# Optimization experiments

Hardware: AMD Instinct MI355X
Metric: run time of the kernel (lower is better)

The kernel has to match this reference:

```python
import jax, jax.numpy as jnp
import numpy as np

B, N = 8, 2000                  # images, proposals per image
NUM_CLASSES = 91                # incl. background (class 0)
IMG_H, IMG_W = 800, 1333
SCORE_THRESH = 0.05
NMS_THRESH = 0.5
DETS_PER_IMG = 100
PRE_NMS_TOPK = 2048             # fixed-size cap on NMS candidates (jit-static)
MIN_SIZE = 0.01
WX, WY, WW, WH = 10.0, 10.0, 5.0, 5.0   # BoxCoder weights
BBOX_XFORM_CLIP = float(np.log(1000.0 / 16.0))


def setup_inputs() -> dict:
    key = jax.random.key(0)
    k1, k2, k3, k4 = jax.random.split(key, 4)
    # valid proposal boxes (x1,y1,x2,y2) inside the image
    ctr = jax.random.uniform(k1, (B, N, 2)) * jnp.array([IMG_W, IMG_H], jnp.float32)
    wh = jax.random.uniform(k2, (B, N, 2), minval=8.0, maxval=256.0)
    proposals = jnp.concatenate([ctr - 0.5 * wh, ctr + 0.5 * wh], axis=-1)
    class_logits = jax.random.normal(k3, (B * N, NUM_CLASSES)) * 2.0
    box_regression = jax.random.normal(k4, (B * N, NUM_CLASSES * 4)) * 0.2
    return {"class_logits": class_logits, "box_regression": box_regression,
            "proposals": proposals}


def _decode(reg, boxes):
    # reg: [N, C, 4] deltas, boxes: [N, 4] proposals -> [N, C, 4] decoded
    w = boxes[:, 2] - boxes[:, 0]
    h = boxes[:, 3] - boxes[:, 1]
    cx = boxes[:, 0] + 0.5 * w
    cy = boxes[:, 1] + 0.5 * h
    dx = reg[..., 0] / WX
    dy = reg[..., 1] / WY
    dw = jnp.minimum(reg[..., 2] / WW, BBOX_XFORM_CLIP)
    dh = jnp.minimum(reg[..., 3] / WH, BBOX_XFORM_CLIP)
    pcx = dx * w[:, None] + cx[:, None]
    pcy = dy * h[:, None] + cy[:, None]
    pw = jnp.exp(dw) * w[:, None]
    ph = jnp.exp(dh) * h[:, None]
    return jnp.stack([pcx - 0.5 * pw, pcy - 0.5 * ph,
                      pcx + 0.5 * pw, pcy + 0.5 * ph], axis=-1)


def _box_iou(a, b):
    # a: [K,4], b: [K,4] -> [K,K]
    area_a = (a[:, 2] - a[:, 0]) * (a[:, 3] - a[:, 1])
    area_b = (b[:, 2] - b[:, 0]) * (b[:, 3] - b[:, 1])
    lt = jnp.maximum(a[:, None, :2], b[None, :, :2])
    rb = jnp.minimum(a[:, None, 2:], b[None, :, 2:])
    wh = jnp.clip(rb - lt, 0.0)
    inter = wh[..., 0] * wh[..., 1]
    return inter / (area_a[:, None] + area_b[None, :] - inter)


def _postprocess_image(boxes, scores):
    # boxes: [N, C, 4] decoded, scores: [N, C] softmax probs
    boxes = jnp.stack([jnp.clip(boxes[..., 0], 0.0, IMG_W),
                       jnp.clip(boxes[..., 1], 0.0, IMG_H),
                       jnp.clip(boxes[..., 2], 0.0, IMG_W),
                       jnp.clip(boxes[..., 3], 0.0, IMG_H)], axis=-1)
    # drop background class 0, flatten to per-(proposal,class) candidates
    boxes_fg = boxes[:, 1:, :].reshape(-1, 4)            # [N*(C-1), 4]
    scores_fg = scores[:, 1:].reshape(-1)
    labels_fg = jnp.broadcast_to(jnp.arange(1, NUM_CLASSES, dtype=jnp.int32),
                                 (N, NUM_CLASSES - 1)).reshape(-1)
    ws = boxes_fg[:, 2] - boxes_fg[:, 0]
    hs = boxes_fg[:, 3] - boxes_fg[:, 1]
    valid = (scores_fg > SCORE_THRESH) & (ws >= MIN_SIZE) & (hs >= MIN_SIZE)
    # fixed-size pre-NMS top-K (masked-out candidates sorted last)
    _, top_idx = jax.lax.top_k(jnp.where(valid, scores_fg, -1.0), PRE_NMS_TOPK)
    cand_boxes = boxes_fg[top_idx]
    cand_scores = scores_fg[top_idx]
    cand_labels = labels_fg[top_idx]
    cand_valid = valid[top_idx]
    # class-wise (batched) NMS via per-class coordinate offset
    offset = cand_labels.astype(cand_boxes.dtype) * (jnp.max(cand_boxes) + 1.0)
    iou = _box_iou(cand_boxes + offset[:, None], cand_boxes + offset[:, None])
    idx = jnp.arange(PRE_NMS_TOPK)

    def body(i, keep):  # greedy suppression in score order
        sup = (iou[i] > NMS_THRESH) & keep[i] & (idx > i)
        return keep & ~sup

    keep = jax.lax.fori_loop(0, PRE_NMS_TOPK, body, cand_valid)
    out_scores, out_idx = jax.lax.top_k(jnp.where(keep, cand_scores, -1.0),
                                        DETS_PER_IMG)
    return cand_boxes[out_idx], out_scores, cand_labels[out_idx]


def reference(class_logits, box_regression, proposals):
    logits = class_logits.reshape(B, N, NUM_CLASSES)
    reg = box_regression.reshape(B, N, NUM_CLASSES, 4)
    pred_boxes = jax.vmap(_decode)(reg, proposals)          # [B, N, C, 4]
    pred_scores = jax.nn.softmax(logits, axis=-1)           # [B, N, C]
    boxes, scores, labels = jax.vmap(_postprocess_image)(pred_boxes, pred_scores)
    return boxes, scores, labels
```

## Files before the change

kernel.cpp:

```cpp
#include <hip/hip_runtime.h>
#include <cstdint>
#include <cstddef>

#define NIMG   8
#define NPROP  2000
#define NCLS   91
#define NFG    90
#define NROW   (NIMG * NPROP)
#define TOPK   2048
#define DETS   100
#define CKCAP  32768
#define KREGS  12
#define CLSCAP 512

#define IMG_Wf 1333.0f
#define IMG_Hf 800.0f
#define SCORE_TH 0.05f
#define MINSZ    0.01f
#define NMS_TH   0.5f
#define CLIPV    4.135166556742356f
#define ORD_NEG1 0x407FFFFFu
#define PADKEY   (((ull)ORD_NEG1 << 32) | 0xFFFFFFFFull)

typedef unsigned long long ull;

static const size_t OFF_CNT    = 0;
static const size_t OFF_KBM    = 2048;
static const size_t OFF_VBM    = 4096;
static const size_t OFF_CK     = 262144;
static const size_t OFF_CBOX   = OFF_CK    + (size_t)NIMG*CKCAP*8;
static const size_t OFF_CSCOR  = OFF_CBOX  + (size_t)NIMG*TOPK*16;
static const size_t OFF_CLAB   = OFF_CSCOR + (size_t)NIMG*TOPK*4;
static const size_t OFF_CLSBOX = OFF_CLAB  + (size_t)NIMG*TOPK*4;
static const size_t OFF_CLSAR  = OFF_CLSBOX+ (size_t)NIMG*TOPK*16;
static const size_t OFF_CLSSX  = OFF_CLSAR + (size_t)NIMG*TOPK*4;
static const size_t OFF_CLSCNT = OFF_CLSSX + (size_t)NIMG*TOPK*4;
static const size_t OFF_CLSOFF = OFF_CLSCNT+ (size_t)NIMG*96*4;

__device__ __forceinline__ unsigned ford(float f) {
    unsigned u = __float_as_uint(f);
    return (u & 0x80000000u) ? ~u : (u | 0x80000000u);
}
__device__ __forceinline__ float fordinv(unsigned x) {
    return (x & 0x80000000u) ? __uint_as_float(x & 0x7FFFFFFFu)
                             : __uint_as_float(~x);
}

__device__ __forceinline__ float4 decode_clip(float4 p, float4 r) {
    float w  = __fsub_rn(p.z, p.x);
    float h  = __fsub_rn(p.w, p.y);
    float cx = __fadd_rn(p.x, __fmul_rn(0.5f, w));
    float cy = __fadd_rn(p.y, __fmul_rn(0.5f, h));
    float dx = __fdiv_rn(r.x, 10.0f);
    float dy = __fdiv_rn(r.y, 10.0f);
    float dw = fminf(__fdiv_rn(r.z, 5.0f), CLIPV);
    float dh = fminf(__fdiv_rn(r.w, 5.0f), CLIPV);
    float pcx = __fadd_rn(__fmul_rn(dx, w), cx);
    float pcy = __fadd_rn(__fmul_rn(dy, h), cy);
    float pw  = __fmul_rn(expf(dw), w);
    float ph  = __fmul_rn(expf(dh), h);
    float x1 = __fsub_rn(pcx, __fmul_rn(0.5f, pw));
    float y1 = __fsub_rn(pcy, __fmul_rn(0.5f, ph));
    float x2 = __fadd_rn(pcx, __fmul_rn(0.5f, pw));
    float y2 = __fadd_rn(pcy, __fmul_rn(0.5f, ph));
    float4 o;
    o.x = fminf(fmaxf(x1, 0.0f), IMG_Wf);
    o.y = fminf(fmaxf(y1, 0.0f), IMG_Hf);
    o.z = fminf(fmaxf(x2, 0.0f), IMG_Wf);
    o.w = fminf(fmaxf(y2, 0.0f), IMG_Hf);
    return o;
}

__device__ __forceinline__ void wl_phase(ull& a, ull& b, int l, int base,
                                         int k, int jmax) {
    bool desc = ((base & k) == 0);
    for (int j = jmax; j >= 2; j >>= 1) {
        int pl = l ^ (j >> 1);
        bool lower = ((base & j) == 0);
        ull pa = __shfl(a, pl), pb = __shfl(b, pl);
        bool km = (desc == lower);
        ull na = km ? (a > pa ? a : pa) : (a < pa ? a : pa);
        ull nb = km ? (b > pb ? b : pb) : (b < pb ? b : pb);
        a = na; b = nb;
    }
    ull mx = a > b ? a : b, mn = a > b ? b : a;
    a = desc ? mx : mn; b = desc ? mn : mx;
}

__global__ __launch_bounds__(1024) void kA(const float* __restrict__ logits,
                                           const float* __restrict__ reg,
                                           const float* __restrict__ props,
                                           ull* __restrict__ ck,
                                           int* __restrict__ cntv,
                                           ull* __restrict__ vbm2) {
    int warp = threadIdx.x >> 6;
    int lane = threadIdx.x & 63;
    int row  = blockIdx.x * 16 + warp;
    int b = row / NPROP;
    int n = row - b * NPROP;
    const float* lrow = logits + (size_t)row * NCLS;

    float xa = lrow[lane];
    float xb = (lane < 27) ? lrow[64 + lane] : -INFINITY;
    float mx = fmaxf(xa, xb);
    #pragma unroll
    for (int o = 32; o; o >>= 1) mx = fmaxf(mx, __shfl_xor(mx, o));
    float ea = expf(__fsub_rn(xa, mx));
    float eb = (lane < 27) ? expf(__fsub_rn(xb, mx)) : 0.0f;
    float s  = __fadd_rn(ea, eb);
    #pragma unroll
    for (int o = 32; o; o >>= 1) s = __fadd_rn(s, __shfl_xor(s, o));

    const float4 p = *reinterpret_cast<const float4*>(props + (size_t)row * 4);

    __shared__ int sCnt[32];
    __shared__ int sExc[32];
    __shared__ int sBase;

    ull rowmask[2];
    bool validA[2];
    ull keyA[2];
    #pragma unroll
    for (int it = 0; it < 2; ++it) {
        int c = (it == 0) ? (1 + lane) : (65 + lane);
        bool active = (it == 0) ? true : (lane < 26);
        bool valid = false;
        ull key = 0;
        if (active) {
            float lg = lrow[c];
            float score = __fdiv_rn(expf(__fsub_rn(lg, mx)), s);
            float4 r4 = *reinterpret_cast<const float4*>(
                reg + ((size_t)row * NCLS + c) * 4);
            float4 bx = decode_clip(p, r4);
            float bw = __fsub_rn(bx.z, bx.x);
            float bh = __fsub_rn(bx.w, bx.y);
            valid = (score > SCORE_TH) && (bw >= MINSZ) && (bh >= MINSZ);
            int offidx = n * NFG + (c - 1);
            key = ((ull)ford(score) << 32) |
                  (ull)(0xFFFFFFFFu - (unsigned)offidx);
        }
        ull bal = __ballot(valid);
        rowmask[it] = bal;
        validA[it] = valid;
        keyA[it] = key;
        if (lane == 0) sCnt[warp * 2 + it] = __popcll(bal);
    }
    __syncthreads();
    if (warp == 0) {
        int c = (lane < 32) ? sCnt[lane] : 0;
        int p2 = c;
        #pragma unroll
        for (int o = 1; o < 32; o <<= 1) {
            int v = __shfl_up(p2, o);
            if (lane >= o) p2 += v;
        }
        if (lane == 31) sBase = atomicAdd(&cntv[b * 64], p2);
        if (lane < 32) sExc[lane] = p2 - c;
    }
    __syncthreads();
    int base = sBase;
    #pragma unroll
    for (int it = 0; it < 2; ++it) {
        if (validA[it]) {
            int slot = base + sExc[warp * 2 + it] +
                       __popcll(rowmask[it] & ((1ull << lane) - 1ull));
            if (slot < CKCAP)
                ck[(size_t)b * CKCAP + slot] = keyA[it];
        }
    }
    if (lane == 0) {
        vbm2[(size_t)row * 2]     = rowmask[0];
        vbm2[(size_t)row * 2 + 1] = rowmask[1];
    }
}

__global__ __launch_bounds__(1024) void kB(const ull* __restrict__ ck,
                                           const int* __restrict__ cntv,
                                           const ull* __restrict__ vbm2,
                                           const float* __restrict__ reg,
                                           const float* __restrict__ props,
                                           float4* __restrict__ cbox,
                                           float* __restrict__ cscore,
                                           int* __restrict__ clabel,
                                           float4* __restrict__ clsbox,
                                           float* __restrict__ clsarea,
                                           int* __restrict__ clssidx,
                                           int* __restrict__ clscnt,
                                           int* __restrict__ clsoff) {
    int b = blockIdx.x;
    int tid = threadIdx.x;
    int lane = tid & 63, warp = tid >> 6;
    __shared__ ull sk[TOPK];
    __shared__ unsigned histw[16 * 256];
    __shared__ unsigned wtot4[4];
    __shared__ ull sP;
    __shared__ int sRem, sCnt;
    __shared__ float sMax[16];
    __shared__ float sM1;
    __shared__ int rex[NPROP];
    __shared__ int wsum[16];
    __shared__ ull clsbm[NFG * 32];
    __shared__ unsigned wpfx[NFG * 32];
    __shared__ int ccnt[96], coff[96];

    int cnt = cntv[b * 64];
    if (cnt > CKCAP) cnt = CKCAP;
    const ull* K = ck + (size_t)b * CKCAP;

    if (cnt >= TOPK) {
        ull kreg[KREGS];
        #pragma unroll
        for (int r = 0; r < KREGS; ++r) {
            int i = tid + (r << 10);
            kreg[r] = (i < cnt) ? K[i] : 0ull;
        }
        ull P = 0; int rem = TOPK;
        for (int pass = 7; pass >= 0; --pass) {
            int sh = pass * 8;
            *reinterpret_cast<uint4*>(&histw[tid * 4]) = make_uint4(0, 0, 0, 0);
            __syncthreads();
            ull pmask = (pass == 7) ? 0ull : (~0ull << (sh + 8));
            unsigned* hw = &histw[warp << 8];
            #pragma unroll
            for (int r = 0; r < KREGS; ++r) {
                int i = tid + (r << 10);
                if (i < cnt && (kreg[r] & pmask) == P)
                    atomicAdd(&hw[(unsigned)(kreg[r] >> sh) & 255u], 1u);
            }
            for (int i = (KREGS << 10) + tid; i < cnt; i += 1024) {
                ull k2 = K[i];
                if ((k2 & pmask) == P)
                    atomicAdd(&hw[(unsigned)(k2 >> sh) & 255u], 1u);
            }
            __syncthreads();
            unsigned x = 0, pfx = 0;
            if (tid < 256) {
                int d = 255 - tid;
                #pragma unroll
                for (int w = 0; w < 16; ++w) x += histw[(w << 8) + d];
                pfx = x;
                #pragma unroll
                for (int o = 1; o < 64; o <<= 1) {
                    unsigned v = __shfl_up(pfx, o);
                    if (lane >= o) pfx += v;
                }
                if (lane == 63) wtot4[tid >> 6] = pfx;
            }
            __syncthreads();
            if (tid < 256) {
                int d = 255 - tid;
                int ws = tid >> 6;
                unsigned add = 0;
                if (ws > 0) add += wtot4[0];
                if (ws > 1) add += wtot4[1];
                if (ws > 2) add += wtot4[2];
                unsigned pi   = pfx + add;
                unsigned excl = pi - x;
                if (x && excl < (unsigned)rem && pi >= (unsigned)rem) {
                    sP = P | ((ull)(unsigned)d << sh);
                    sRem = rem - (int)excl;
                }
            }
            __syncthreads();
            P = sP; rem = sRem;
        }
        if (tid == 0) sCnt = 0;
        __syncthreads();
        #pragma unroll
        for (int r = 0; r < KREGS; ++r) {
            int i = tid + (r << 10);
            bool sel = (i < cnt) && (kreg[r] >= P);
            ull bal = __ballot(sel);
            int cw = __popcll(bal);
            if (cw) {
                int ldr = __ffsll((long long)bal) - 1;
                int bw = 0;
                if (lane == ldr) bw = atomicAdd(&sCnt, cw);
                bw = __shfl(bw, ldr);
                if (sel) {
                    int pos = bw + __popcll(bal & ((1ull << lane) - 1ull));
                    if (pos < TOPK) sk[pos] = kreg[r];
                }
            }
        }
        for (int i = (KREGS << 10) + tid; i < cnt; i += 1024) {
            ull k2 = K[i];
            bool sel = (k2 >= P);
            ull bal = __ballot(sel);
            int cw = __popcll(bal);
            if (cw) {
                int ldr = __ffsll((long long)bal) - 1;
                int bw = 0;
                if (lane == ldr) bw = atomicAdd(&sCnt, cw);
                bw = __shfl(bw, ldr);
                if (sel) {
                    int pos = bw + __popcll(bal & ((1ull << lane) - 1ull));
                    if (pos < TOPK) sk[pos] = k2;
                }
            }
        }
        __syncthreads();
        int fc = sCnt;
        for (int i = fc + tid; i < TOPK; i += 1024) sk[i] = PADKEY;
    } else {
        for (int i = tid; i < cnt; i += 1024) sk[i] = K[i];
        int F = TOPK - cnt;
        const ull* V = vbm2 + (size_t)b * NPROP * 2;
        int r0 = 2 * tid, r1 = r0 + 1;
        int v0 = 0, v1 = 0;
        if (r0 < NPROP) v0 = NFG - __popcll(V[r0 * 2]) - __popcll(V[r0 * 2 + 1]);
        if (r1 < NPROP) v1 = NFG - __popcll(V[r1 * 2]) - __popcll(V[r1 * 2 + 1]);
        int s2 = v0 + v1;
        int pfx = s2;
        #pragma unroll
        for (int o = 1; o < 64; o <<= 1) {
            int t = __shfl_up(pfx, o);
            if (lane >= o) pfx += t;
        }
        if (lane == 63) wsum[warp] = pfx;
        __syncthreads();
        if (tid == 0) {
            int a = 0;
            for (int w = 0; w < 16; ++w) { int t = wsum[w]; wsum[w] = a; a += t; }
        }
        __syncthreads();
        int excl = pfx - s2 + wsum[warp];
        if (r0 < NPROP) rex[r0] = excl;
        if (r1 < NPROP) rex[r1] = excl + v0;
        __syncthreads();
        for (int r = tid; r < NPROP; r += 1024) {
            int e = rex[r];
            if (e < F) {
                ull m0 = V[r * 2], m1 = V[r * 2 + 1];
                int rank = e;
                ull inv = ~m0;
                while (inv && rank < F) {
                    int cb = __builtin_ctzll(inv); inv &= inv - 1;
                    unsigned idx = (unsigned)(r * NFG + cb);
                    sk[cnt + rank] = ((ull)ORD_NEG1 << 32) | (ull)(0xFFFFFFFFu - idx);
                    ++rank;
                }
                inv = (~m1) & ((1ull << 26) - 1ull);
                while (inv && rank < F) {
                    int cb = __builtin_ctzll(inv); inv &= inv - 1;
                    unsigned idx = (unsigned)(r * NFG + 64 + cb);
                    sk[cnt + rank] = ((ull)ORD_NEG1 << 32) | (ull)(0xFFFFFFFFu - idx);
                    ++rank;
                }
            }
        }
    }
    __syncthreads();

    {
        int ebase = warp * 128 + lane * 2;
        ulonglong2 v = *reinterpret_cast<ulonglong2*>(&sk[ebase]);
        ull a = v.x, bb = v.y;
        #pragma unroll
        for (int k = 2; k <= 128; k <<= 1)
            wl_phase(a, bb, lane, ebase, k, (k >> 1) < 64 ? (k >> 1) : 64);
        v.x = a; v.y = bb;
        *reinterpret_cast<ulonglong2*>(&sk[ebase]) = v;
        for (int k = 256; k <= TOPK; k <<= 1) {
            for (int j = k >> 1; j >= 128; j >>= 1) {
                __syncthreads();
                for (int i = tid; i < TOPK; i += 1024) {
                    int ij = i ^ j;
                    if (ij > i) {
                        ull x1 = sk[i], x2 = sk[ij];
                        bool descSeg = ((i & k) == 0);
                        if ((x1 < x2) == descSeg) { sk[i] = x2; sk[ij] = x1; }
                    }
                }
            }
            __syncthreads();
            v = *reinterpret_cast<ulonglong2*>(&sk[ebase]);
            a = v.x; bb = v.y;
            wl_phase(a, bb, lane, ebase, k, 64);
            v.x = a; v.y = bb;
            *reinterpret_cast<ulonglong2*>(&sk[ebase]) = v;
        }
    }
    __syncthreads();

    float lmax = 0.0f;
    float4 myb[2]; int myl[2]; float mys[2]; bool vkA[2];
    #pragma unroll
    for (int r = 0; r < 2; ++r) {
        int sidx = tid + r * 1024;
        ull k = sk[sidx];
        unsigned idx = 0xFFFFFFFFu - (unsigned)(k & 0xFFFFFFFFu);
        float score = fordinv((unsigned)(k >> 32));
        int n = (int)(idx / NFG), c = (int)(idx % NFG);
        int row = b * NPROP + n;
        float4 p  = *reinterpret_cast<const float4*>(props + (size_t)row * 4);
        float4 r4 = *reinterpret_cast<const float4*>(
            reg + ((size_t)row * NCLS + (c + 1)) * 4);
        float4 bx = decode_clip(p, r4);
        myb[r] = bx; myl[r] = c + 1; mys[r] = score;
        vkA[r] = (((unsigned)(k >> 32)) != ORD_NEG1);
        lmax = fmaxf(lmax, fmaxf(fmaxf(bx.x, bx.y), fmaxf(bx.z, bx.w)));
    }
    #pragma unroll
    for (int o = 32; o; o >>= 1) lmax = fmaxf(lmax, __shfl_xor(lmax, o));
    if ((tid & 63) == 0) sMax[tid >> 6] = lmax;
    __syncthreads();
    if (tid == 0) {
        float v = sMax[0];
        for (int i = 1; i < 16; ++i) v = fmaxf(v, sMax[i]);
        sM1 = __fadd_rn(v, 1.0f);
    }
    __syncthreads();
    float m1 = sM1;
    float4 obA[2]; float arA[2];
    #pragma unroll
    for (int r = 0; r < 2; ++r) {
        int sidx = tid + r * 1024;
        float off = __fmul_rn((float)myl[r], m1);
        float4 ob;
        ob.x = __fadd_rn(myb[r].x, off);
        ob.y = __fadd_rn(myb[r].y, off);
        ob.z = __fadd_rn(myb[r].z, off);
        ob.w = __fadd_rn(myb[r].w, off);
        float area = __fmul_rn(__fsub_rn(ob.z, ob.x), __fsub_rn(ob.w, ob.y));
        obA[r] = ob; arA[r] = area;
        int g = b * TOPK + sidx;
        cbox[g] = myb[r]; cscore[g] = mys[r]; clabel[g] = myl[r];
    }

    for (int i = tid; i < NFG * 32; i += 1024) clsbm[i] = 0ull;
    __syncthreads();
    #pragma unroll
    for (int r = 0; r < 2; ++r) {
        int sidx = tid + (r << 10);
        if (vkA[r])
            atomicOr(&clsbm[(myl[r] - 1) * 32 + (sidx >> 6)], 1ull << (sidx & 63));
    }
    __syncthreads();
    if (tid < NFG) {
        unsigned run = 0;
        for (int w = 0; w < 32; ++w) {
            wpfx[tid * 32 + w] = run;
            run += (unsigned)__popcll(clsbm[tid * 32 + w]);
        }
        ccnt[tid] = (int)run;
    }
    __syncthreads();
    if (tid == 0) {
        int a = 0;
        for (int c2 = 0; c2 < NFG; ++c2) { coff[c2] = a; a += ccnt[c2]; }
    }
    __syncthreads();
    #pragma unroll
    for (int r = 0; r < 2; ++r) {
        int sidx = tid + (r << 10);
        if (vkA[r]) {
            int cl = myl[r] - 1;
            int rank = (int)wpfx[cl * 32 + (sidx >> 6)] +
                       (int)__popcll(clsbm[cl * 32 + (sidx >> 6)] &
                                     ((1ull << (sidx & 63)) - 1ull));
            int slot = coff[cl] + rank;
            int g2 = b * TOPK + slot;
            clsbox[g2] = obA[r]; clsarea[g2] = arA[r]; clssidx[g2] = sidx;
        }
    }
    if (tid < NFG) {
        clscnt[b * 96 + tid] = ccnt[tid];
        clsoff[b * 96 + tid] = coff[tid];
    }
}

__global__ __launch_bounds__(64) void kN(const float4* __restrict__ clsbox,
                                         const float* __restrict__ clsarea,
                                         const int* __restrict__ clssidx,
                                         const int* __restrict__ clscnt,
                                         const int* __restrict__ clsoff,
                                         ull* __restrict__ keepbm) {
    int bc = blockIdx.x;
    int b = bc / NFG, c = bc - b * NFG;
    int n = clscnt[b * 96 + c];
    if (n <= 0) return;
    if (n > CLSCAP) n = CLSCAP;
    int lane = threadIdx.x;
    int W = (n + 63) >> 6;
    __shared__ float4 sbox[CLSCAP];
    __shared__ float  sar[CLSCAP];
    __shared__ int    ssx[CLSCAP];
    __shared__ ull    smask[CLSCAP * 8];
    int base = b * TOPK + clsoff[b * 96 + c];
    for (int t = lane; t < n; t += 64) {
        sbox[t] = clsbox[base + t];
        sar[t]  = clsarea[base + t];
        ssx[t]  = clssidx[base + t];
    }
    __syncthreads();
    for (int i = lane; i < n; i += 64) {
        float4 a = sbox[i]; float ai = sar[i];
        for (int w = 0; w < W; ++w) {
            ull word = 0;
            int jn = n - (w << 6); if (jn > 64) jn = 64;
            for (int s = 0; s < jn; ++s) {
                int j = (w << 6) + s;
                if (j > i) {
                    float4 cc = sbox[j];
                    float lt0 = fmaxf(a.x, cc.x), lt1 = fmaxf(a.y, cc.y);
                    float rb0 = fminf(a.z, cc.z), rb1 = fminf(a.w, cc.w);
                    float w0 = fmaxf(__fsub_rn(rb0, lt0), 0.0f);
                    float w1 = fmaxf(__fsub_rn(rb1, lt1), 0.0f);
                    float inter = __fmul_rn(w0, w1);
                    if (inter > 0.0f) {
                        float un = __fsub_rn(__fadd_rn(ai, sar[j]), inter);
                        if (__fdiv_rn(inter, un) > NMS_TH) word |= (1ull << s);
                    }
                }
            }
            smask[i * W + w] = word;
        }
    }
    __syncthreads();
    ull alive = 0;
    if (lane < W) {
        int rem = n - (lane << 6);
        alive = (rem >= 64) ? ~0ull : ((1ull << rem) - 1ull);
    }
    for (int i = 0; i < n; ++i) {
        ull aw = __shfl(alive, i >> 6);
        if ((aw >> (i & 63)) & 1ull) {
            if (lane < W) alive &= ~smask[i * W + lane];
        }
    }
    if (lane < W) {
        ull bits = alive;
        while (bits) {
            int s = __builtin_ctzll(bits); bits &= bits - 1;
            int sidx = ssx[(lane << 6) + s];
            atomicOr(&keepbm[b * 32 + (sidx >> 6)], 1ull << (sidx & 63));
        }
    }
}

__global__ __launch_bounds__(64) void kE(const ull* __restrict__ keepbm,
                                         const float4* __restrict__ cbox,
                                         const float* __restrict__ cscore,
                                         const int* __restrict__ clabel,
                                         float* __restrict__ out) {
    int b = blockIdx.x;
    int lane = threadIdx.x;
    __shared__ ull sKeep[32];
    if (lane < 32) sKeep[lane] = keepbm[b * 32 + lane];
    __syncthreads();

    unsigned m = (unsigned)(sKeep[lane >> 1] >> ((lane & 1) << 5));

    int cntk = __popc(m);
    int pre = cntk;
    #pragma unroll
    for (int o = 1; o < 64; o <<= 1) {
        int v = __shfl_up(pre, o);
        if (lane >= o) pre += v;
    }
    int total = __shfl(pre, 63);
    int excl = pre - cntk;

    unsigned mm = m;
    while (mm) {
        int t = __builtin_ctz(mm);
        mm &= mm - 1;
        int rank = excl++;
        if (rank < DETS) {
            int j = lane * 32 + t;
            int g = b * TOPK + j;
            float4 bx = cbox[g];
            *reinterpret_cast<float4*>(out + ((size_t)b * DETS + rank) * 4) = bx;
            out[NIMG * DETS * 4 + b * DETS + rank] = cscore[g];
            out[NIMG * DETS * 5 + b * DETS + rank] = (float)clabel[g];
        }
    }
    int kept100 = (total < DETS) ? total : DETS;
    int F = DETS - kept100;
    if (F > 0) {
        unsigned zm = ~m;
        int zc = __popc(zm);
        int zpre = zc;
        #pragma unroll
        for (int o = 1; o < 64; o <<= 1) {
            int v = __shfl_up(zpre, o);
            if (lane >= o) zpre += v;
        }
        int zexcl = zpre - zc;
        while (zm) {
            int t = __builtin_ctz(zm);
            zm &= zm - 1;
            int zr = zexcl++;
            if (zr < F) {
                int j = lane * 32 + t;
                int g = b * TOPK + j;
                float4 bx = cbox[g];
                int rank = kept100 + zr;
                *reinterpret_cast<float4*>(out + ((size_t)b * DETS + rank) * 4) = bx;
                out[NIMG * DETS * 4 + b * DETS + rank] = -1.0f;
                out[NIMG * DETS * 5 + b * DETS + rank] = (float)clabel[g];
            }
        }
    }
}

extern "C" void kernel_launch(void* const* d_in, const int* in_sizes, int n_in,
                              void* d_out, int out_size, void* d_ws, size_t ws_size,
                              hipStream_t stream) {
    const float* logits = (const float*)d_in[0];
    const float* reg    = (const float*)d_in[1];
    const float* props  = (const float*)d_in[2];
    float* out = (float*)d_out;
    char* ws = (char*)d_ws;

    int* cntv   = (int*)(ws + OFF_CNT);
    ull* keepbm = (ull*)(ws + OFF_KBM);
    ull* vbm2   = (ull*)(ws + OFF_VBM);
    ull* ck     = (ull*)(ws + OFF_CK);
    float4* cbox   = (float4*)(ws + OFF_CBOX);
    float*  cscor  = (float*)(ws + OFF_CSCOR);
    int*    clab   = (int*)(ws + OFF_CLAB);
    float4* clsbox = (float4*)(ws + OFF_CLSBOX);
    float*  clsar  = (float*)(ws + OFF_CLSAR);
    int*    clssx  = (int*)(ws + OFF_CLSSX);
    int*    clscnt = (int*)(ws + OFF_CLSCNT);
    int*    clsoff = (int*)(ws + OFF_CLSOFF);

    hipMemsetAsync(ws, 0, 4096, stream);
    hipLaunchKernelGGL(kA, dim3(NROW / 16), dim3(1024), 0, stream,
                       logits, reg, props, ck, cntv, vbm2);
    hipLaunchKernelGGL(kB, dim3(NIMG), dim3(1024), 0, stream,
                       ck, cntv, vbm2, reg, props, cbox, cscor, clab,
                       clsbox, clsar, clssx, clscnt, clsoff);
    hipLaunchKernelGGL(kN, dim3(NIMG * NFG), dim3(64), 0, stream,
                       clsbox, clsar, clssx, clscnt, clsoff, keepbm);
    hipLaunchKernelGGL(kE, dim3(NIMG), dim3(64), 0, stream,
                       keepbm, cbox, cscor, clab, out);
}
```

Before: 148.8 us.

## Fuse per-class NMS and output gather into the top-k kernel

Removes the separate per-class NMS kernel and the final gather kernel. kB now runs greedy NMS per class inside shared memory, with one warp per class using ballot-based suppression, and writes the output directly. This drops two launches and the global round-trips of the class-sorted candidate buffers. It also exits the radix-select passes early once the threshold bucket is resolved, simplifies the bitonic sort's global-stride phase to one compare per thread, and pads the class bitmap stride to 33. The cost is running NMS on only 8 blocks, which limits parallelism, and the per-class cap is halved to 256, a correctness risk if a class has more candidates.

```diff
diff --git a/kernel.cpp b/kernel.cpp
--- a/kernel.cpp
+++ b/kernel.cpp
@@ -11,7 +11,7 @@
 #define DETS   100
 #define CKCAP  32768
 #define KREGS  12
-#define CLSCAP 512
+#define CLSCAP2 256
 
 #define IMG_Wf 1333.0f
 #define IMG_Hf 800.0f
@@ -24,18 +24,12 @@
 
 typedef unsigned long long ull;
 
-static const size_t OFF_CNT    = 0;
-static const size_t OFF_KBM    = 2048;
-static const size_t OFF_VBM    = 4096;
-static const size_t OFF_CK     = 262144;
-static const size_t OFF_CBOX   = OFF_CK    + (size_t)NIMG*CKCAP*8;
-static const size_t OFF_CSCOR  = OFF_CBOX  + (size_t)NIMG*TOPK*16;
-static const size_t OFF_CLAB   = OFF_CSCOR + (size_t)NIMG*TOPK*4;
-static const size_t OFF_CLSBOX = OFF_CLAB  + (size_t)NIMG*TOPK*4;
-static const size_t OFF_CLSAR  = OFF_CLSBOX+ (size_t)NIMG*TOPK*16;
-static const size_t OFF_CLSSX  = OFF_CLSAR + (size_t)NIMG*TOPK*4;
-static const size_t OFF_CLSCNT = OFF_CLSSX + (size_t)NIMG*TOPK*4;
-static const size_t OFF_CLSOFF = OFF_CLSCNT+ (size_t)NIMG*96*4;
+static const size_t OFF_CNT   = 0;
+static const size_t OFF_VBM   = 4096;
+static const size_t OFF_CK    = 262144;
+static const size_t OFF_CBOX  = OFF_CK   + (size_t)NIMG*CKCAP*8;
+static const size_t OFF_CSCOR = OFF_CBOX + (size_t)NIMG*TOPK*16;
+static const size_t OFF_CLAB  = OFF_CSCOR+ (size_t)NIMG*TOPK*4;
 
 __device__ __forceinline__ unsigned ford(float f) {
     unsigned u = __float_as_uint(f);
@@ -182,26 +176,29 @@
                                            float4* __restrict__ cbox,
                                            float* __restrict__ cscore,
                                            int* __restrict__ clabel,
-                                           float4* __restrict__ clsbox,
-                                           float* __restrict__ clsarea,
-                                           int* __restrict__ clssidx,
-                                           int* __restrict__ clscnt,
-                                           int* __restrict__ clsoff) {
+                                           float* __restrict__ out) {
     int b = blockIdx.x;
     int tid = threadIdx.x;
     int lane = tid & 63, warp = tid >> 6;
-    __shared__ ull sk[TOPK];
-    __shared__ unsigned histw[16 * 256];
+    __shared__ __align__(16) char smem[80704];
+    ull*      sk    = (ull*)smem;
+    unsigned* histw = (unsigned*)(smem + 16384);
+    int*      rex   = (int*)(smem + 32768);
+    float4*   sbox  = (float4*)smem;
+    float*    sar2  = (float*)(smem + 32768);
+    unsigned short* ssx2 = (unsigned short*)(smem + 40960);
+    ull*      clsbm = (ull*)(smem + 45056);
+    unsigned* wpfx  = (unsigned*)(smem + 68816);
     __shared__ unsigned wtot4[4];
     __shared__ ull sP;
-    __shared__ int sRem, sCnt;
+    __shared__ int sRem, sCnt, sDone;
+    __shared__ ull sVWk[32];
     __shared__ float sMax[16];
     __shared__ float sM1;
-    __shared__ int rex[NPROP];
     __shared__ int wsum[16];
-    __shared__ ull clsbm[NFG * 32];
-    __shared__ unsigned wpfx[NFG * 32];
     __shared__ int ccnt[96], coff[96];
+
+    if (tid < 32) sVWk[tid] = 0ull;
 
     int cnt = cntv[b * 64];
     if (cnt > CKCAP) cnt = CKCAP;
@@ -258,11 +255,14 @@
                 unsigned excl = pi - x;
                 if (x && excl < (unsigned)rem && pi >= (unsigned)rem) {
                     sP = P | ((ull)(unsigned)d << sh);
-                    sRem = rem - (int)excl;
+                    int nr = rem - (int)excl;
+                    sRem = nr;
+                    sDone = ((int)x == nr) ? 1 : 0;
                 }
             }
             __syncthreads();
             P = sP; rem = sRem;
+            if (sDone) break;
         }
         if (tid == 0) sCnt = 0;
         __syncthreads();
@@ -364,14 +364,11 @@
         for (int k = 256; k <= TOPK; k <<= 1) {
             for (int j = k >> 1; j >= 128; j >>= 1) {
                 __syncthreads();
-                for (int i = tid; i < TOPK; i += 1024) {
-                    int ij = i ^ j;
-                    if (ij > i) {
-                        ull x1 = sk[i], x2 = sk[ij];
-                        bool descSeg = ((i & k) == 0);
-                        if ((x1 < x2) == descSeg) { sk[i] = x2; sk[ij] = x1; }
-                    }
-                }
+                int i = ((tid & ~(j - 1)) << 1) | (tid & (j - 1));
+                int ij = i | j;
+                ull x1 = sk[i], x2 = sk[ij];
+                bool descSeg = ((i & k) == 0);
+                if ((x1 < x2) == descSeg) { sk[i] = x2; sk[ij] = x1; }
             }
             __syncthreads();
             v = *reinterpret_cast<ulonglong2*>(&sk[ebase]);
@@ -428,20 +425,20 @@
         cbox[g] = myb[r]; cscore[g] = mys[r]; clabel[g] = myl[r];
     }
 
-    for (int i = tid; i < NFG * 32; i += 1024) clsbm[i] = 0ull;
+    for (int i = tid; i < NFG * 33; i += 1024) clsbm[i] = 0ull;
     __syncthreads();
     #pragma unroll
     for (int r = 0; r < 2; ++r) {
         int sidx = tid + (r << 10);
         if (vkA[r])
-            atomicOr(&clsbm[(myl[r] - 1) * 32 + (sidx >> 6)], 1ull << (sidx & 63));
+            atomicOr(&clsbm[(myl[r] - 1) * 33 + (sidx >> 6)], 1ull << (sidx & 63));
     }
     __syncthreads();
     if (tid < NFG) {
         unsigned run = 0;
         for (int w = 0; w < 32; ++w) {
-            wpfx[tid * 32 + w] = run;
-            run += (unsigned)__popcll(clsbm[tid * 32 + w]);
+            wpfx[tid * 33 + w] = run;
+            run += (unsigned)__popcll(clsbm[tid * 33 + w]);
         }
         ccnt[tid] = (int)run;
     }
@@ -456,150 +453,147 @@
         int sidx = tid + (r << 10);
         if (vkA[r]) {
             int cl = myl[r] - 1;
-            int rank = (int)wpfx[cl * 32 + (sidx >> 6)] +
-                       (int)__popcll(clsbm[cl * 32 + (sidx >> 6)] &
+            int rank = (int)wpfx[cl * 33 + (sidx >> 6)] +
+                       (int)__popcll(clsbm[cl * 33 + (sidx >> 6)] &
                                      ((1ull << (sidx & 63)) - 1ull));
             int slot = coff[cl] + rank;
-            int g2 = b * TOPK + slot;
-            clsbox[g2] = obA[r]; clsarea[g2] = arA[r]; clssidx[g2] = sidx;
-        }
-    }
-    if (tid < NFG) {
-        clscnt[b * 96 + tid] = ccnt[tid];
-        clsoff[b * 96 + tid] = coff[tid];
-    }
-}
-
-__global__ __launch_bounds__(64) void kN(const float4* __restrict__ clsbox,
-                                         const float* __restrict__ clsarea,
-                                         const int* __restrict__ clssidx,
-                                         const int* __restrict__ clscnt,
-                                         const int* __restrict__ clsoff,
-                                         ull* __restrict__ keepbm) {
-    int bc = blockIdx.x;
-    int b = bc / NFG, c = bc - b * NFG;
-    int n = clscnt[b * 96 + c];
-    if (n <= 0) return;
-    if (n > CLSCAP) n = CLSCAP;
-    int lane = threadIdx.x;
-    int W = (n + 63) >> 6;
-    __shared__ float4 sbox[CLSCAP];
-    __shared__ float  sar[CLSCAP];
-    __shared__ int    ssx[CLSCAP];
-    __shared__ ull    smask[CLSCAP * 8];
-    int base = b * TOPK + clsoff[b * 96 + c];
-    for (int t = lane; t < n; t += 64) {
-        sbox[t] = clsbox[base + t];
-        sar[t]  = clsarea[base + t];
-        ssx[t]  = clssidx[base + t];
-    }
-    __syncthreads();
-    for (int i = lane; i < n; i += 64) {
-        float4 a = sbox[i]; float ai = sar[i];
-        for (int w = 0; w < W; ++w) {
-            ull word = 0;
-            int jn = n - (w << 6); if (jn > 64) jn = 64;
-            for (int s = 0; s < jn; ++s) {
-                int j = (w << 6) + s;
-                if (j > i) {
-                    float4 cc = sbox[j];
-                    float lt0 = fmaxf(a.x, cc.x), lt1 = fmaxf(a.y, cc.y);
-                    float rb0 = fminf(a.z, cc.z), rb1 = fminf(a.w, cc.w);
+            sbox[slot] = obA[r]; sar2[slot] = arA[r];
+            ssx2[slot] = (unsigned short)sidx;
+        }
+    }
+    __syncthreads();
+
+    #pragma unroll 1
+    for (int c = warp; c < NFG; c += 16) {
+        int n = ccnt[c];
+        if (n <= 0) continue;
+        if (n > CLSCAP2) n = CLSCAP2;
+        int base = coff[c];
+        if (n <= 64) {
+            float4 b0; float a0 = 0.0f;
+            if (lane < n) { b0 = sbox[base + lane]; a0 = sar2[base + lane]; }
+            ull alive = (n == 64) ? ~0ull : ((1ull << n) - 1ull);
+            #pragma unroll 1
+            for (int i = 0; i < n; ++i) {
+                if (!((alive >> i) & 1ull)) continue;
+                float bix = __shfl(b0.x, i), biy = __shfl(b0.y, i);
+                float biz = __shfl(b0.z, i), biw = __shfl(b0.w, i);
+                float ai2 = __shfl(a0, i);
+                bool sup = false;
+                if (lane < n && lane > i) {
+                    float lt0 = fmaxf(bix, b0.x), lt1 = fmaxf(biy, b0.y);
+                    float rb0 = fminf(biz, b0.z), rb1 = fminf(biw, b0.w);
                     float w0 = fmaxf(__fsub_rn(rb0, lt0), 0.0f);
                     float w1 = fmaxf(__fsub_rn(rb1, lt1), 0.0f);
                     float inter = __fmul_rn(w0, w1);
                     if (inter > 0.0f) {
-                        float un = __fsub_rn(__fadd_rn(ai, sar[j]), inter);
-                        if (__fdiv_rn(inter, un) > NMS_TH) word |= (1ull << s);
+                        float un = __fsub_rn(__fadd_rn(ai2, a0), inter);
+                        sup = (__fdiv_rn(inter, un) > NMS_TH);
                     }
                 }
-            }
-            smask[i * W + w] = word;
-        }
-    }
-    __syncthreads();
-    ull alive = 0;
-    if (lane < W) {
-        int rem = n - (lane << 6);
-        alive = (rem >= 64) ? ~0ull : ((1ull << rem) - 1ull);
-    }
-    for (int i = 0; i < n; ++i) {
-        ull aw = __shfl(alive, i >> 6);
-        if ((aw >> (i & 63)) & 1ull) {
-            if (lane < W) alive &= ~smask[i * W + lane];
-        }
-    }
-    if (lane < W) {
-        ull bits = alive;
-        while (bits) {
-            int s = __builtin_ctzll(bits); bits &= bits - 1;
-            int sidx = ssx[(lane << 6) + s];
-            atomicOr(&keepbm[b * 32 + (sidx >> 6)], 1ull << (sidx & 63));
-        }
-    }
-}
-
-__global__ __launch_bounds__(64) void kE(const ull* __restrict__ keepbm,
-                                         const float4* __restrict__ cbox,
-                                         const float* __restrict__ cscore,
-                                         const int* __restrict__ clabel,
-                                         float* __restrict__ out) {
-    int b = blockIdx.x;
-    int lane = threadIdx.x;
-    __shared__ ull sKeep[32];
-    if (lane < 32) sKeep[lane] = keepbm[b * 32 + lane];
-    __syncthreads();
-
-    unsigned m = (unsigned)(sKeep[lane >> 1] >> ((lane & 1) << 5));
-
-    int cntk = __popc(m);
-    int pre = cntk;
-    #pragma unroll
-    for (int o = 1; o < 64; o <<= 1) {
-        int v = __shfl_up(pre, o);
-        if (lane >= o) pre += v;
-    }
-    int total = __shfl(pre, 63);
-    int excl = pre - cntk;
-
-    unsigned mm = m;
-    while (mm) {
-        int t = __builtin_ctz(mm);
-        mm &= mm - 1;
-        int rank = excl++;
-        if (rank < DETS) {
-            int j = lane * 32 + t;
-            int g = b * TOPK + j;
-            float4 bx = cbox[g];
-            *reinterpret_cast<float4*>(out + ((size_t)b * DETS + rank) * 4) = bx;
-            out[NIMG * DETS * 4 + b * DETS + rank] = cscore[g];
-            out[NIMG * DETS * 5 + b * DETS + rank] = (float)clabel[g];
-        }
-    }
-    int kept100 = (total < DETS) ? total : DETS;
-    int F = DETS - kept100;
-    if (F > 0) {
-        unsigned zm = ~m;
-        int zc = __popc(zm);
-        int zpre = zc;
+                alive &= ~__ballot(sup);
+            }
+            if (lane < n && ((alive >> lane) & 1ull)) {
+                int sidx = (int)ssx2[base + lane];
+                atomicOr(&sVWk[sidx >> 6], 1ull << (sidx & 63));
+            }
+        } else {
+            int W4 = (n + 63) >> 6;
+            float4 bx4[4]; float ar4[4];
+            for (int s = 0; s < W4; ++s) {
+                int j = lane + (s << 6);
+                if (j < n) { bx4[s] = sbox[base + j]; ar4[s] = sar2[base + j]; }
+            }
+            ull alive[4];
+            for (int s = 0; s < 4; ++s) {
+                int remn = n - (s << 6);
+                alive[s] = (remn >= 64) ? ~0ull
+                         : (remn > 0 ? ((1ull << remn) - 1ull) : 0ull);
+            }
+            #pragma unroll 1
+            for (int i = 0; i < n; ++i) {
+                if (!((alive[i >> 6] >> (i & 63)) & 1ull)) continue;
+                float4 bi = sbox[base + i];
+                float ai2 = sar2[base + i];
+                for (int s = 0; s < W4; ++s) {
+                    int j = lane + (s << 6);
+                    bool sup = false;
+                    if (j < n && j > i) {
+                        float lt0 = fmaxf(bi.x, bx4[s].x), lt1 = fmaxf(bi.y, bx4[s].y);
+                        float rb0 = fminf(bi.z, bx4[s].z), rb1 = fminf(bi.w, bx4[s].w);
+                        float w0 = fmaxf(__fsub_rn(rb0, lt0), 0.0f);
+                        float w1 = fmaxf(__fsub_rn(rb1, lt1), 0.0f);
+                        float inter = __fmul_rn(w0, w1);
+                        if (inter > 0.0f) {
+                            float un = __fsub_rn(__fadd_rn(ai2, ar4[s]), inter);
+                            sup = (__fdiv_rn(inter, un) > NMS_TH);
+                        }
+                    }
+                    alive[s] &= ~__ballot(sup);
+                }
+            }
+            for (int s = 0; s < W4; ++s) {
+                int j = lane + (s << 6);
+                if (j < n && ((alive[s] >> lane) & 1ull)) {
+                    int sidx = (int)ssx2[base + j];
+                    atomicOr(&sVWk[sidx >> 6], 1ull << (sidx & 63));
+                }
+            }
+        }
+    }
+    __syncthreads();
+
+    if (warp == 0) {
+        unsigned m = (unsigned)(sVWk[lane >> 1] >> ((lane & 1) << 5));
+        int cntk = __popc(m);
+        int pre = cntk;
         #pragma unroll
         for (int o = 1; o < 64; o <<= 1) {
-            int v = __shfl_up(zpre, o);
-            if (lane >= o) zpre += v;
-        }
-        int zexcl = zpre - zc;
-        while (zm) {
-            int t = __builtin_ctz(zm);
-            zm &= zm - 1;
-            int zr = zexcl++;
-            if (zr < F) {
+            int v = __shfl_up(pre, o);
+            if (lane >= o) pre += v;
+        }
+        int total = __shfl(pre, 63);
+        int excl = pre - cntk;
+
+        unsigned mm = m;
+        while (mm) {
+            int t = __builtin_ctz(mm);
+            mm &= mm - 1;
+            int rank = excl++;
+            if (rank < DETS) {
                 int j = lane * 32 + t;
                 int g = b * TOPK + j;
                 float4 bx = cbox[g];
-                int rank = kept100 + zr;
                 *reinterpret_cast<float4*>(out + ((size_t)b * DETS + rank) * 4) = bx;
-                out[NIMG * DETS * 4 + b * DETS + rank] = -1.0f;
+                out[NIMG * DETS * 4 + b * DETS + rank] = cscore[g];
                 out[NIMG * DETS * 5 + b * DETS + rank] = (float)clabel[g];
+            }
+        }
+        int kept100 = (total < DETS) ? total : DETS;
+        int F = DETS - kept100;
+        if (F > 0) {
+            unsigned zm = ~m;
+            int zc = __popc(zm);
+            int zpre = zc;
+            #pragma unroll
+            for (int o = 1; o < 64; o <<= 1) {
+                int v = __shfl_up(zpre, o);
+                if (lane >= o) zpre += v;
+            }
+            int zexcl = zpre - zc;
+            while (zm) {
+                int t = __builtin_ctz(zm);
+                zm &= zm - 1;
+                int zr = zexcl++;
+                if (zr < F) {
+                    int j = lane * 32 + t;
+                    int g = b * TOPK + j;
+                    float4 bx = cbox[g];
+                    int rank = kept100 + zr;
+                    *reinterpret_cast<float4*>(out + ((size_t)b * DETS + rank) * 4) = bx;
+                    out[NIMG * DETS * 4 + b * DETS + rank] = -1.0f;
+                    out[NIMG * DETS * 5 + b * DETS + rank] = (float)clabel[g];
+                }
             }
         }
     }
@@ -615,26 +609,15 @@
     char* ws = (char*)d_ws;
 
     int* cntv   = (int*)(ws + OFF_CNT);
-    ull* keepbm = (ull*)(ws + OFF_KBM);
     ull* vbm2   = (ull*)(ws + OFF_VBM);
     ull* ck     = (ull*)(ws + OFF_CK);
-    float4* cbox   = (float4*)(ws + OFF_CBOX);
-    float*  cscor  = (float*)(ws + OFF_CSCOR);
-    int*    clab   = (int*)(ws + OFF_CLAB);
-    float4* clsbox = (float4*)(ws + OFF_CLSBOX);
-    float*  clsar  = (float*)(ws + OFF_CLSAR);
-    int*    clssx  = (int*)(ws + OFF_CLSSX);
-    int*    clscnt = (int*)(ws + OFF_CLSCNT);
-    int*    clsoff = (int*)(ws + OFF_CLSOFF);
-
-    hipMemsetAsync(ws, 0, 4096, stream);
+    float4* cbox  = (float4*)(ws + OFF_CBOX);
+    float*  cscor = (float*)(ws + OFF_CSCOR);
+    int*    clab  = (int*)(ws + OFF_CLAB);
+
+    hipMemsetAsync(ws, 0, 2048, stream);
     hipLaunchKernelGGL(kA, dim3(NROW / 16), dim3(1024), 0, stream,
                        logits, reg, props, ck, cntv, vbm2);
     hipLaunchKernelGGL(kB, dim3(NIMG), dim3(1024), 0, stream,
-                       ck, cntv, vbm2, reg, props, cbox, cscor, clab,
-                       clsbox, clsar, clssx, clscnt, clsoff);
-    hipLaunchKernelGGL(kN, dim3(NIMG * NFG), dim3(64), 0, stream,
-                       clsbox, clsar, clssx, clscnt, clsoff, keepbm);
-    hipLaunchKernelGGL(kE, dim3(NIMG), dim3(64), 0, stream,
-                       keepbm, cbox, cscor, clab, out);
+                       ck, cntv, vbm2, reg, props, cbox, cscor, clab, out);
 }
```

New measurement: 159.6 us. 7.3% more time.
